# Kernel optimization log

Measured on AMD Instinct MI355X. Metric: run time of the kernel, lower is better.

## Reference

```python
import jax, jax.numpy as jnp
from jax import lax
import numpy as np


def setup_inputs() -> dict:
    key = jax.random.key(0)
    T, W = 2048, 30  # document length, max span width
    starts = jnp.repeat(jnp.arange(T, dtype=jnp.int32), W)      # [T*W]
    widths = jnp.tile(jnp.arange(W, dtype=jnp.int32), T)        # [T*W]
    ends = jnp.minimum(starts + widths, T - 1)
    spans = jnp.stack([starts, ends], axis=1)                   # [N,2], N=61440
    N = spans.shape[0]
    scores = jax.random.normal(key, (N,), dtype=jnp.float32)
    mask = jnp.ones((N,), dtype=jnp.float32)
    return {
        "spans": spans,
        "span_mention_scores": scores,
        "span_mask": mask,
        "token_num": T,
        "num_spans_to_keep": int(0.4 * T),
    }


def _greedy_non_crossing(spans, scores, mask, T, k):
    """Greedy NMS-style selection of up to k spans with no crossing overlap.
    Faithful to masked_topk_non_overlap: iterate candidates in descending
    (score + log(mask)) order; a candidate (s,e) is rejected iff it crosses
    an already-selected span, tracked via start_to_max_end / end_to_min_start
    tables. Sequential dependence expressed as lax.scan; the O(span_width)
    inner token loop is vectorized as an O(T) masked range query.
    """
    N = scores.shape[0]
    order = jnp.argsort(-(scores + jnp.log(mask)))  # descending sort
    starts = spans[:, 0].astype(jnp.int32)
    ends = spans[:, 1].astype(jnp.int32)
    tok = jnp.arange(T, dtype=jnp.int32)

    def step(carry, c):
        s2e, e2s, sel, cnt = carry
        s = starts[c]
        e = ends[c]
        # token_idx in (s, e] with start_to_max_end[token_idx] > e -> crossing
        cross1 = jnp.any((tok > s) & (tok <= e) & (s2e > e))
        # token_idx in [s, e) with 0 <= end_to_min_start[token_idx] < s -> crossing
        cross2 = jnp.any((tok >= s) & (tok < e) & (e2s >= 0) & (e2s < s))
        accept = jnp.logical_and(jnp.logical_not(cross1 | cross2), cnt < k)
        # start_to_max_end[s] = max(old, e) if accepted
        s2e = s2e.at[s].set(jnp.where(accept, jnp.maximum(s2e[s], e), s2e[s]))
        # end_to_min_start[e] = s if unset or s smaller, if accepted
        cur = e2s[e]
        e2s = e2s.at[e].set(jnp.where(accept & ((cur == -1) | (s < cur)), s, cur))
        sel = sel.at[c].set(sel[c] | accept)
        cnt = cnt + accept.astype(jnp.int32)
        return (s2e, e2s, sel, cnt), None

    init = (jnp.full((T,), -1, dtype=jnp.int32),
            jnp.full((T,), -1, dtype=jnp.int32),
            jnp.zeros((N,), dtype=bool),
            jnp.int32(0))
    (s2e, e2s, sel, cnt), _ = lax.scan(step, init, order)

    # sort selected candidates by (start, end); pad to fixed size k
    sort_key = jnp.where(sel, starts * T + ends, T * T)  # T*T > any valid key
    idx = jnp.argsort(sort_key)[:k]
    valid = jnp.arange(k) < cnt
    top_idx = jnp.where(valid, idx, 0)
    return top_idx, valid


def reference(spans, span_mention_scores, span_mask, token_num, num_spans_to_keep):
    top_idx, valid = _greedy_non_crossing(
        spans, span_mention_scores, span_mask, token_num, num_spans_to_keep)
    top_scores = jnp.where(valid, span_mention_scores[top_idx], 0.0)
    top_spans = jnp.where(valid[:, None], spans[top_idx], 0)
    return top_scores, top_idx, top_spans, valid
```

## Files before the change

kernel.cpp:

```cpp
#include <hip/hip_runtime.h>
#include <math.h>
#include <limits.h>

#define TPB   1024
#define TILE  1024
#define MAXT  2048
#define TPAD  64
#define MAXK  1024
#define MAXW  29
#define BATCH 1024
#define FLAGSTRIDE 16

struct SortSM {
  union {
    unsigned h[4 * 256];
    unsigned wcnt[16][256];
  };
  unsigned baseL[256];
};

__device__ inline void gbar(unsigned* ctr, int idx, unsigned nblk) {
  __syncthreads();
  if (threadIdx.x == 0) {
    __threadfence();
    atomicAdd(&ctr[idx], 1u);
    while (atomicAdd(&ctr[idx], 0u) < nblk) { __builtin_amdgcn_s_sleep(8); }
    __threadfence();
  }
  __syncthreads();
}

__global__ void __launch_bounds__(TPB, 4) sort_kernel(
    const float* __restrict__ scores, const float* __restrict__ mask,
    int N, int nT, unsigned* ctr, unsigned* pflag, unsigned* ghist,
    unsigned* tileCnt, unsigned* keysA, unsigned* keysB, int* idxA, int* idxB) {
  __shared__ SortSM s;
  __shared__ unsigned base4[4][256];
  const int tid = threadIdx.x;
  const int lane = tid & 63;
  const int wave = tid >> 6;

  if (tid < 1024) s.h[tid] = 0;
  __syncthreads();
  {
    int i = blockIdx.x * TILE + tid;
    if (i < N) {
      float kf = scores[i] + logf(mask[i]);
      unsigned u = __float_as_uint(kf);
      u = (u & 0x80000000u) ? ~u : (u | 0x80000000u);
      u = ~u;
      keysA[i] = u;
      atomicAdd(&s.h[(u & 255u)], 1u);
      atomicAdd(&s.h[256 + ((u >> 8) & 255u)], 1u);
      atomicAdd(&s.h[512 + ((u >> 16) & 255u)], 1u);
      atomicAdd(&s.h[768 + (u >> 24)], 1u);
    }
    __syncthreads();
    if (tid < 1024 && s.h[tid]) atomicAdd(&ghist[tid], s.h[tid]);
  }
  gbar(ctr, 0, nT);

  if (wave < 4) {
    const int p = wave;
    unsigned v0 = ghist[p * 256 + 4 * lane + 0];
    unsigned v1 = ghist[p * 256 + 4 * lane + 1];
    unsigned v2 = ghist[p * 256 + 4 * lane + 2];
    unsigned v3 = ghist[p * 256 + 4 * lane + 3];
    unsigned sum = v0 + v1 + v2 + v3;
    unsigned x = sum;
    for (int off = 1; off < 64; off <<= 1) {
      unsigned y = __shfl_up(x, off, 64);
      if (lane >= off) x += y;
    }
    unsigned excl = x - sum;
    base4[p][4 * lane + 0] = excl;
    base4[p][4 * lane + 1] = excl + v0;
    base4[p][4 * lane + 2] = excl + v0 + v1;
    base4[p][4 * lane + 3] = excl + v0 + v1 + v2;
  }
  __syncthreads();

  for (int p = 0; p < 4; ++p) {
    const unsigned* srck = (p & 1) ? keysB : keysA;
    const int*      srci = (p & 1) ? idxB : idxA;
    unsigned*       dstk = (p & 1) ? keysA : keysB;
    int*            dsti = (p & 1) ? idxA : idxB;
    const int shift = 8 * p;
    unsigned* flg = pflag + p * nT * FLAGSTRIDE;

    for (int j = tid; j < 16 * 256; j += TPB)
      (&s.wcnt[0][0])[j] = 0;
    __syncthreads();

    int i = blockIdx.x * TILE + tid;
    bool v = (i < N);
    unsigned key = v ? srck[i] : 0u;
    int pay = v ? ((p == 0) ? i : srci[i]) : 0;
    unsigned d = (key >> shift) & 255u;
    unsigned long long mm = __ballot(v);
    #pragma unroll
    for (int b = 0; b < 8; ++b) {
      unsigned long long bb = __ballot((d >> b) & 1u);
      mm &= ((d >> b) & 1u) ? bb : ~bb;
    }
    unsigned rnk = (unsigned)__popcll(mm & ((1ull << lane) - 1ull));
    if (v && rnk == 0) s.wcnt[wave][d] = (unsigned)__popcll(mm);
    __syncthreads();
    if (tid < 256) {
      unsigned run = 0;
      #pragma unroll
      for (int g = 0; g < 16; ++g) {
        unsigned c = s.wcnt[g][tid];
        s.wcnt[g][tid] = run;
        run += c;
      }
      tileCnt[blockIdx.x * 256 + tid] = run;
    }
    __syncthreads();

    if (tid == 0) {
      __threadfence();
      atomicExch(&flg[blockIdx.x * FLAGSTRIDE], 1u);
    }
    if (tid < blockIdx.x) {
      while (atomicAdd(&flg[tid * FLAGSTRIDE], 0u) == 0u)
        __builtin_amdgcn_s_sleep(2);
    }
    __syncthreads();
    if (tid == 0) __threadfence();
    __syncthreads();

    if (tid < 256) {
      unsigned baseacc = base4[p][tid];
      for (int t = 0; t < blockIdx.x; ++t)
        baseacc += tileCnt[t * 256 + tid];
      s.baseL[tid] = baseacc;
    }
    __syncthreads();
    if (v) {
      unsigned pos = s.baseL[d] + s.wcnt[wave][d] + rnk;
      dstk[pos] = key;
      dsti[pos] = pay;
    }
    if (p < 3) gbar(ctr, 1 + p, nT);
  }
}

__device__ inline bool precheck30(const unsigned* tabP, int cc, int cs, int ce) {
  if (cc < 0) return false;
  int w = ce - cs;
  bool crossed = false;
  #pragma unroll
  for (int off = 0; off <= MAXW; ++off) {
    unsigned tv = tabP[cs + off];
    crossed |= ((off >= 1) & (off <= w) & ((tv & 0xFFFFu) > (unsigned)(ce + 1)))
             | ((off < w) & ((tv >> 16) < (unsigned)cs));
  }
  for (int off = MAXW + 1; off <= w; ++off) {
    unsigned tv = tabP[cs + off];
    crossed |= ((tv & 0xFFFFu) > (unsigned)(ce + 1));
    if (off < w) crossed |= ((tv >> 16) < (unsigned)cs);
  }
  return !crossed;
}

__global__ void __launch_bounds__(TPB, 4) greedy_kernel(
    const int2* __restrict__ spans2, const int* __restrict__ spans,
    const float* __restrict__ scores, const int* __restrict__ order,
    const int* __restrict__ tnum_p, const int* __restrict__ keep_p,
    float* __restrict__ out, int N) {
  __shared__ unsigned tabP[MAXT + TPAD];
  __shared__ int2 tab[MAXT + TPAD];
  __shared__ unsigned long long acc[MAXK];
  __shared__ unsigned long long surv[BATCH];
  __shared__ unsigned long long Cmat[BATCH];
  __shared__ int wvs[16];
  __shared__ int gcnt;

  const int tid = threadIdx.x;
  const int lane = tid & 63;
  const int wave = tid >> 6;
  const int T  = tnum_p[0];
  const int k0 = keep_p[0];
  const int k  = (k0 < MAXK) ? k0 : MAXK;

  for (int t = tid; t < MAXT + TPAD; t += TPB) {
    tab[t] = make_int2(-1, INT_MAX);
    tabP[t] = 0xFFFF0000u;
  }
  if (tid == 0) gcnt = 0;
  __syncthreads();

  int cc = -1, cs = 0, ce = 0, nn = -1;
  if (tid < N)         cc = order[tid];
  if (BATCH + tid < N) nn = order[BATCH + tid];
  if (cc >= 0) { int2 sp = spans2[cc]; cs = sp.x; ce = sp.y; }

  int cnt = 0;
  for (int c0 = 0; c0 < N && cnt < k; c0 += BATCH) {
    int pc = nn, ps = 0, pe = 0;
    if (pc >= 0) { int2 sp = spans2[pc]; ps = sp.x; pe = sp.y; }
    int i2 = c0 + 2 * BATCH + tid;
    nn = (i2 < N) ? order[i2] : -1;

    bool ok = precheck30(tabP, cc, cs, ce);
    unsigned long long bal = __ballot(ok);
    if (lane == 0) wvs[wave] = (int)__popcll(bal);
    __syncthreads();
    int ns = 0, wb = 0;
    #pragma unroll
    for (int w2 = 0; w2 < 16; ++w2) {
      if (w2 == wave) wb = ns;
      ns += wvs[w2];
    }

    if (ns > 0) {
      if (ok) {
        int pos = wb + (int)__popcll(bal & ((1ull << lane) - 1ull));
        surv[pos] = ((unsigned long long)(unsigned)cs << 48)
                  | ((unsigned long long)(unsigned)ce << 32)
                  | (unsigned)cc;
      }
      __syncthreads();

      for (int v = tid; v < ns; v += TPB) {
        unsigned long long pk = surv[v];
        int gs = (int)(pk >> 48), ge = (int)((pk >> 32) & 0xFFFFu);
        int gbase = v & ~63;
        int m = ns - gbase; if (m > 64) m = 64;
        unsigned long long C = 0;
        for (int j = 0; j < m; ++j) {
          unsigned long long pj = surv[gbase + j];
          int sj = (int)(pj >> 48), ej = (int)((pj >> 32) & 0xFFFFu);
          bool cr = (gs < sj && sj <= ge && ej > ge) ||
                    (sj < gs && gs <= ej && ej < ge);
          C |= (unsigned long long)cr << j;
        }
        Cmat[v] = C;
      }
      __syncthreads();

      if (tid < 64) {
        bool dirty = false;
        for (int g = 0; g < ns && cnt < k; g += 64) {
          int m = ns - g; if (m > 64) m = 64;
          bool act = lane < m;
          int gs = 0, ge = 0, gc = 0;
          unsigned long long C = 0;
          if (act) {
            unsigned long long pk = surv[g + lane];
            gs = (int)(pk >> 48);
            ge = (int)((pk >> 32) & 0xFFFFu);
            gc = (int)(unsigned)pk;
            C  = Cmat[g + lane];
          }
          bool pre = act;
          if (dirty) {
            pre = act && precheck30(tabP, gc, gs, ge);
          }
          unsigned long long preB = __ballot(pre);
          if (preB == 0ull) continue;
          int np = (int)__popcll(preB);
          unsigned long long lower = (1ull << lane) - 1ull;
          unsigned long long accm;
          int cnt0g = cnt;
          if (np == 1) {
            accm = preB;
            cnt += 1;
          } else {
            unsigned long long Cl = C & lower;
            unsigned long long resolvedB = ~preB;
            accm = 0ull;
            while (true) {
              bool meUn   = ((resolvedB >> lane) & 1ull) == 0ull;
              bool killed = (Cl & accm) != 0ull;
              bool ready  = (Cl & ~resolvedB) == 0ull;
              unsigned long long newacc = __ballot(meUn && ready && !killed);
              unsigned long long newrej = __ballot(meUn && killed);
              if (!(newacc | newrej)) break;
              accm |= newacc;
              resolvedB |= (newacc | newrej);
            }
            int nacc = (int)__popcll(accm);
            if (cnt + nacc > k) {
              int room = k - cnt;
              bool a0 = ((accm >> lane) & 1ull) != 0ull;
              int ar = (int)__popcll(accm & lower);
              accm = __ballot(a0 && (ar < room));
              nacc = room;
            }
            cnt += nacc;
          }
          bool accme = ((accm >> lane) & 1ull) != 0ull;
          if (accme) {
            int rank = (int)__popcll(accm & lower);
            acc[cnt0g + rank] =
                ((unsigned long long)(unsigned)(gs * T + ge) << 32) | (unsigned)gc;
            atomicMax(&tab[gs].x, ge);
            atomicMin(&tab[ge].y, gs);
          }
          if (accme) {
            int2 tv = tab[gs];
            tabP[gs] = ((unsigned)(tv.y > 65535 ? 65535 : tv.y) << 16)
                     | (unsigned)(tv.x + 1);
            int2 tv2 = tab[ge];
            tabP[ge] = ((unsigned)(tv2.y > 65535 ? 65535 : tv2.y) << 16)
                     | (unsigned)(tv2.x + 1);
          }
          if (accm) dirty = true;
        }
        if (lane == 0) gcnt = cnt;
      }
      __syncthreads();
      cnt = gcnt;
    }

    cc = pc; cs = ps; ce = pe;
  }

  int M = 2;
  while (M < cnt) M <<= 1;
  for (int j = tid; j < M; j += TPB)
    if (j >= cnt) acc[j] = ~0ull;
  __syncthreads();
  for (int kk = 2; kk <= M; kk <<= 1) {
    for (int jj = kk >> 1; jj > 0; jj >>= 1) {
      for (int i3 = tid; i3 < M; i3 += TPB) {
        int ixj = i3 ^ jj;
        if (ixj > i3) {
          unsigned long long a = acc[i3], b = acc[ixj];
          bool up = ((i3 & kk) == 0);
          if ((a > b) == up) { acc[i3] = b; acc[ixj] = a; }
        }
      }
      __syncthreads();
    }
  }

  for (int j = tid; j < k0; j += TPB) {
    if (j < cnt) {
      int cand = (int)(acc[j] & 0xFFFFFFFFu);
      out[j]                  = scores[cand];
      out[k0 + j]             = (float)cand;
      out[2 * k0 + 2 * j]     = (float)spans[2 * cand];
      out[2 * k0 + 2 * j + 1] = (float)spans[2 * cand + 1];
      out[4 * k0 + j]         = 1.0f;
    } else {
      out[j]                  = 0.0f;
      out[k0 + j]             = 0.0f;
      out[2 * k0 + 2 * j]     = 0.0f;
      out[2 * k0 + 2 * j + 1] = 0.0f;
      out[4 * k0 + j]         = 0.0f;
    }
  }
}

extern "C" void kernel_launch(void* const* d_in, const int* in_sizes, int n_in,
                              void* d_out, int out_size, void* d_ws, size_t ws_size,
                              hipStream_t stream) {
  const int*   spans  = (const int*)d_in[0];
  const float* scores = (const float*)d_in[1];
  const float* mask   = (const float*)d_in[2];
  const int*   tnum   = (const int*)d_in[3];
  const int*   keep   = (const int*)d_in[4];
  const int N = in_sizes[1];
  const int nT = (N + TILE - 1) / TILE;

  unsigned* ctr     = (unsigned*)d_ws;
  unsigned* pflag   = ctr + 32;
  unsigned* ghist   = pflag + (size_t)4 * nT * FLAGSTRIDE;
  unsigned* tileCnt = ghist + 1024;
  unsigned* keysA   = tileCnt + (size_t)nT * 256;
  unsigned* keysB   = keysA + N;
  int*      idxA    = (int*)(keysB + N);
  int*      idxB    = idxA + N;
  float*    out     = (float*)d_out;

  hipMemsetAsync(ctr, 0,
                 (32 + (size_t)4 * nT * FLAGSTRIDE + 1024) * sizeof(unsigned),
                 stream);

  sort_kernel<<<nT, TPB, 0, stream>>>(scores, mask, N, nT, ctr, pflag, ghist,
                                      tileCnt, keysA, keysB, idxA, idxB);
  greedy_kernel<<<1, TPB, 0, stream>>>((const int2*)spans, spans, scores,
                                       idxA, tnum, keep, out, N);
}
```

Measured before the change: 237.9 us.

## Fuse sort and greedy kernels; replace counter barriers with per-block flag barriers

Merges the radix sort kernel and the single-block greedy kernel into one launch. After the sort, block 0 waits on per-block completion flags and then runs the greedy selection, while the other blocks exit. The global barriers move from one atomic counter polled with atomicAdd to per-block flags polled with acquire loads, with an occasional atomic fallback. This removes one kernel launch gap and cuts contention on a single barrier counter. In exchange, shared memory use rises because both phases' arrays now live in one kernel, which may limit occupancy, and it adds more flag memory to clear with the memset.

Result: slower. 245.9 us (+3.4%).

```diff
diff --git a/kernel.cpp b/kernel.cpp
--- a/kernel.cpp
+++ b/kernel.cpp
@@ -19,21 +19,52 @@
   unsigned baseL[256];
 };
 
-__device__ inline void gbar(unsigned* ctr, int idx, unsigned nblk) {
+__device__ inline void dbar(unsigned* flg, int nblk) {
   __syncthreads();
   if (threadIdx.x == 0) {
     __threadfence();
-    atomicAdd(&ctr[idx], 1u);
-    while (atomicAdd(&ctr[idx], 0u) < nblk) { __builtin_amdgcn_s_sleep(8); }
-    __threadfence();
-  }
+    atomicExch(&flg[blockIdx.x * FLAGSTRIDE], 1u);
+  }
+  if ((int)threadIdx.x < nblk) {
+    int spin = 0;
+    while (__hip_atomic_load(&flg[threadIdx.x * FLAGSTRIDE], __ATOMIC_ACQUIRE,
+                             __HIP_MEMORY_SCOPE_AGENT) == 0u) {
+      __builtin_amdgcn_s_sleep(2);
+      if ((++spin & 255) == 0) {
+        if (atomicAdd(&flg[threadIdx.x * FLAGSTRIDE], 0u) != 0u) break;
+      }
+    }
+  }
+  __syncthreads();
+  if (threadIdx.x == 0) __threadfence();
   __syncthreads();
 }
 
-__global__ void __launch_bounds__(TPB, 4) sort_kernel(
-    const float* __restrict__ scores, const float* __restrict__ mask,
-    int N, int nT, unsigned* ctr, unsigned* pflag, unsigned* ghist,
-    unsigned* tileCnt, unsigned* keysA, unsigned* keysB, int* idxA, int* idxB) {
+__device__ inline bool precheck30(const unsigned* tabP, int cc, int cs, int ce) {
+  if (cc < 0) return false;
+  int w = ce - cs;
+  bool crossed = false;
+  #pragma unroll
+  for (int off = 0; off <= MAXW; ++off) {
+    unsigned tv = tabP[cs + off];
+    crossed |= ((off >= 1) & (off <= w) & ((tv & 0xFFFFu) > (unsigned)(ce + 1)))
+             | ((off < w) & ((tv >> 16) < (unsigned)cs));
+  }
+  for (int off = MAXW + 1; off <= w; ++off) {
+    unsigned tv = tabP[cs + off];
+    crossed |= ((tv & 0xFFFFu) > (unsigned)(ce + 1));
+    if (off < w) crossed |= ((tv >> 16) < (unsigned)cs);
+  }
+  return !crossed;
+}
+
+__global__ void __launch_bounds__(TPB, 4) fused_kernel(
+    const int* __restrict__ spans, const float* __restrict__ scores,
+    const float* __restrict__ mask, const int* __restrict__ tnum_p,
+    const int* __restrict__ keep_p, float* __restrict__ out, int N, int nT,
+    unsigned* pflag, unsigned* ghist, unsigned* tileCnt,
+    unsigned* keysA, unsigned* keysB, int* idxA, int* idxB) {
+  const int2* spans2 = (const int2*)spans;
   __shared__ SortSM s;
   __shared__ unsigned base4[4][256];
   const int tid = threadIdx.x;
@@ -58,7 +89,7 @@
     __syncthreads();
     if (tid < 1024 && s.h[tid]) atomicAdd(&ghist[tid], s.h[tid]);
   }
-  gbar(ctr, 0, nT);
+  dbar(pflag + 0 * nT * FLAGSTRIDE, nT);
 
   if (wave < 4) {
     const int p = wave;
@@ -86,7 +117,7 @@
     unsigned*       dstk = (p & 1) ? keysA : keysB;
     int*            dsti = (p & 1) ? idxA : idxB;
     const int shift = 8 * p;
-    unsigned* flg = pflag + p * nT * FLAGSTRIDE;
+    unsigned* lbf = pflag + (1 + p) * nT * FLAGSTRIDE;
 
     for (int j = tid; j < 16 * 256; j += TPB)
       (&s.wcnt[0][0])[j] = 0;
@@ -120,11 +151,17 @@
 
     if (tid == 0) {
       __threadfence();
-      atomicExch(&flg[blockIdx.x * FLAGSTRIDE], 1u);
+      atomicExch(&lbf[blockIdx.x * FLAGSTRIDE], 1u);
     }
     if (tid < blockIdx.x) {
-      while (atomicAdd(&flg[tid * FLAGSTRIDE], 0u) == 0u)
+      int spin = 0;
+      while (__hip_atomic_load(&lbf[tid * FLAGSTRIDE], __ATOMIC_ACQUIRE,
+                               __HIP_MEMORY_SCOPE_AGENT) == 0u) {
         __builtin_amdgcn_s_sleep(2);
+        if ((++spin & 255) == 0) {
+          if (atomicAdd(&lbf[tid * FLAGSTRIDE], 0u) != 0u) break;
+        }
+      }
     }
     __syncthreads();
     if (tid == 0) __threadfence();
@@ -142,33 +179,35 @@
       dstk[pos] = key;
       dsti[pos] = pay;
     }
-    if (p < 3) gbar(ctr, 1 + p, nT);
-  }
-}
-
-__device__ inline bool precheck30(const unsigned* tabP, int cc, int cs, int ce) {
-  if (cc < 0) return false;
-  int w = ce - cs;
-  bool crossed = false;
-  #pragma unroll
-  for (int off = 0; off <= MAXW; ++off) {
-    unsigned tv = tabP[cs + off];
-    crossed |= ((off >= 1) & (off <= w) & ((tv & 0xFFFFu) > (unsigned)(ce + 1)))
-             | ((off < w) & ((tv >> 16) < (unsigned)cs));
-  }
-  for (int off = MAXW + 1; off <= w; ++off) {
-    unsigned tv = tabP[cs + off];
-    crossed |= ((tv & 0xFFFFu) > (unsigned)(ce + 1));
-    if (off < w) crossed |= ((tv >> 16) < (unsigned)cs);
-  }
-  return !crossed;
-}
-
-__global__ void __launch_bounds__(TPB, 4) greedy_kernel(
-    const int2* __restrict__ spans2, const int* __restrict__ spans,
-    const float* __restrict__ scores, const int* __restrict__ order,
-    const int* __restrict__ tnum_p, const int* __restrict__ keep_p,
-    float* __restrict__ out, int N) {
+    if (p < 3) {
+      dbar(pflag + (5 + p) * nT * FLAGSTRIDE, nT);
+    }
+  }
+
+  {
+    unsigned* fin = pflag + 8 * nT * FLAGSTRIDE;
+    __syncthreads();
+    if (tid == 0) {
+      __threadfence();
+      atomicExch(&fin[blockIdx.x * FLAGSTRIDE], 1u);
+    }
+    if (blockIdx.x != 0) return;
+    if (tid < nT) {
+      int spin = 0;
+      while (__hip_atomic_load(&fin[tid * FLAGSTRIDE], __ATOMIC_ACQUIRE,
+                               __HIP_MEMORY_SCOPE_AGENT) == 0u) {
+        __builtin_amdgcn_s_sleep(2);
+        if ((++spin & 255) == 0) {
+          if (atomicAdd(&fin[tid * FLAGSTRIDE], 0u) != 0u) break;
+        }
+      }
+    }
+    __syncthreads();
+    if (tid == 0) __threadfence();
+    __syncthreads();
+  }
+
+  const int* order = idxA;
   __shared__ unsigned tabP[MAXT + TPAD];
   __shared__ int2 tab[MAXT + TPAD];
   __shared__ unsigned long long acc[MAXK];
@@ -177,9 +216,6 @@
   __shared__ int wvs[16];
   __shared__ int gcnt;
 
-  const int tid = threadIdx.x;
-  const int lane = tid & 63;
-  const int wave = tid >> 6;
   const int T  = tnum_p[0];
   const int k0 = keep_p[0];
   const int k  = (k0 < MAXK) ? k0 : MAXK;
@@ -366,9 +402,8 @@
   const int N = in_sizes[1];
   const int nT = (N + TILE - 1) / TILE;
 
-  unsigned* ctr     = (unsigned*)d_ws;
-  unsigned* pflag   = ctr + 32;
-  unsigned* ghist   = pflag + (size_t)4 * nT * FLAGSTRIDE;
+  unsigned* pflag   = (unsigned*)d_ws;
+  unsigned* ghist   = pflag + (size_t)9 * nT * FLAGSTRIDE;
   unsigned* tileCnt = ghist + 1024;
   unsigned* keysA   = tileCnt + (size_t)nT * 256;
   unsigned* keysB   = keysA + N;
@@ -376,12 +411,11 @@
   int*      idxB    = idxA + N;
   float*    out     = (float*)d_out;
 
-  hipMemsetAsync(ctr, 0,
-                 (32 + (size_t)4 * nT * FLAGSTRIDE + 1024) * sizeof(unsigned),
+  hipMemsetAsync(pflag, 0,
+                 ((size_t)9 * nT * FLAGSTRIDE + 1024) * sizeof(unsigned),
                  stream);
 
-  sort_kernel<<<nT, TPB, 0, stream>>>(scores, mask, N, nT, ctr, pflag, ghist,
-                                      tileCnt, keysA, keysB, idxA, idxB);
-  greedy_kernel<<<1, TPB, 0, stream>>>((const int2*)spans, spans, scores,
-                                       idxA, tnum, keep, out, N);
+  fused_kernel<<<nT, TPB, 0, stream>>>(spans, scores, mask, tnum, keep, out,
+                                       N, nT, pflag, ghist, tileCnt,
+                                       keysA, keysB, idxA, idxB);
 }
```
